# Optimization experiments

Measured on AMD Instinct MI355X. Metric: run time of the kernel, lower is better.

Reference implementation:

```python
import jax, jax.numpy as jnp
import numpy as np

N, D, P = 8192, 512, 3
TEMP, SIM_TH, DIS_TH, CLIP = 0.1, 0.15, 0.35, 30.0
NEG = -1e9  # finite stand-in for -inf mask (exp underflows to 0 identically)


def setup_inputs() -> dict:
    key = jax.random.key(0)
    k1, k2 = jax.random.split(key)
    embeddings = jax.random.normal(k1, (N, D), dtype=jnp.float32)
    thetas = jax.random.uniform(k2, (N, P), dtype=jnp.float32)
    return {"embeddings": embeddings, "thetas": thetas}


def reference(embeddings, thetas):
    n = embeddings.shape[0]
    # F.normalize(dim=-1)
    e = embeddings / jnp.maximum(
        jnp.linalg.norm(embeddings, axis=-1, keepdims=True), 1e-12)
    sim = jnp.clip(e @ e.T / TEMP, -CLIP, CLIP)  # [N, N]

    # cdist(thetas, thetas) normalized by its max; only feeds boolean masks
    t = jax.lax.stop_gradient(thetas)
    sq = jnp.sum(t * t, axis=1)
    d2 = jnp.maximum(sq[:, None] + sq[None, :] - 2.0 * (t @ t.T), 0.0)
    dist = jnp.sqrt(d2)
    dist = dist / (dist.max() + 1e-8)

    eye = jnp.eye(n, dtype=bool)
    pos = (dist < SIM_TH) & ~eye      # positives (self excluded: diag is -inf masked)
    neg = dist > DIS_TH               # negatives (diag never included: dist==0)
    sel = pos | neg

    # per-row cross_entropy over logits [pos_idx; neg_idx] with label 0 is:
    #   -sim[i, first_pos_index(i)] + logsumexp_{j in sel(i)} sim[i, j]
    masked = jnp.where(sel, sim, NEG)
    denom = jax.nn.logsumexp(masked, axis=1)            # [N]
    tgt = jnp.argmax(pos, axis=1)                       # first positive index
    tgt_logit = jnp.take_along_axis(sim, tgt[:, None], axis=1)[:, 0]
    valid = pos.any(axis=1) & neg.any(axis=1)
    per_row = jnp.where(valid, denom - tgt_logit, 0.0)
    cnt = valid.sum()
    return jnp.where(cnt > 0, per_row.sum() / jnp.maximum(cnt, 1), 0.0)
```

## Files before the change

kernel.cpp:

```cpp
#include <hip/hip_runtime.h>

#define N 8192
#define D 512

typedef __attribute__((ext_vector_type(4))) float f32x4;
typedef __attribute__((ext_vector_type(2))) long long2v;

typedef const __attribute__((address_space(1))) unsigned int* gas_t;
typedef __attribute__((address_space(3))) unsigned int* las_t;

static __device__ __forceinline__ void gl_lds16(const void* g, char* l) {
    __builtin_amdgcn_global_load_lds((gas_t)g, (las_t)l, 16, 0, 0);
}
static __device__ __forceinline__ int tri_cum(int r) { return r * (129 - r) / 2; }

static __device__ __forceinline__ unsigned f2fp8(float f) {
    unsigned u = __float_as_uint(f);
    unsigned sgn = (u >> 24) & 0x80u;
    unsigned a = u & 0x7FFFFFFFu;
    if (a >= 0x3C800000u) {
        unsigned t = a + 0x7FFFFu + ((a >> 20) & 1u);
        unsigned code = (((t >> 23) - 120u) << 3) | ((t >> 20) & 7u);
        if (code > 0x7Eu) code = 0x7Eu;
        return sgn | code;
    }
    float af = __uint_as_float(a);
    unsigned m = (unsigned)(af * 512.0f + 0.5f);
    return sgn | (m > 8u ? 8u : m);
}
static __device__ __forceinline__ float fp82f(unsigned c) {
    unsigned e = (c >> 3) & 15u, m = c & 7u;
    float v = (e == 0u) ? (float)m * 0.001953125f
                        : __uint_as_float(((e + 120u) << 23) | (m << 20));
    return (c & 0x80u) ? -v : v;
}

__global__ void knorm(const float* __restrict__ emb, unsigned char* __restrict__ e,
                      float* __restrict__ srow, unsigned* __restrict__ jminrow,
                      unsigned* __restrict__ negrow, unsigned* __restrict__ d2mb) {
    int w    = threadIdx.x >> 6;
    int row  = blockIdx.x * 4 + w;
    int lane = threadIdx.x & 63;
    const float4* src = (const float4*)(emb + (size_t)row * D);
    float4 v0 = src[lane * 2];
    float4 v1 = src[lane * 2 + 1];
    float ss = v0.x*v0.x + v0.y*v0.y + v0.z*v0.z + v0.w*v0.w
             + v1.x*v1.x + v1.y*v1.y + v1.z*v1.z + v1.w*v1.w;
#pragma unroll
    for (int off = 1; off < 64; off <<= 1) ss += __shfl_xor(ss, off, 64);
    float inv = 3.7982826f / fmaxf(sqrtf(ss), 1e-12f);
    unsigned c0 = f2fp8(v0.x * inv), c1 = f2fp8(v0.y * inv);
    unsigned c2 = f2fp8(v0.z * inv), c3 = f2fp8(v0.w * inv);
    unsigned c4 = f2fp8(v1.x * inv), c5 = f2fp8(v1.y * inv);
    unsigned c6 = f2fp8(v1.z * inv), c7 = f2fp8(v1.w * inv);
    uint2 pk;
    pk.x = c0 | (c1 << 8) | (c2 << 16) | (c3 << 24);
    pk.y = c4 | (c5 << 8) | (c6 << 16) | (c7 << 24);
    {
        int c = lane >> 3, u = lane & 7;
        int off8 = c * 64 + ((u < 4) ? u * 16 : (u - 4) * 16 + 8);
        *(uint2*)(e + (size_t)row * D + off8) = pk;
    }
    if (lane == 0) {
        srow[row] = 0.0f;
        jminrow[row] = 0xFFFFFFFFu;
        negrow[row] = 0u;
    }
    if (blockIdx.x == 0 && threadIdx.x == 0) *d2mb = 0u;
}

__global__ void kth(const float* __restrict__ th, float4* __restrict__ th4,
                    unsigned* __restrict__ d2mb) {
    int tid = threadIdx.x, bid = blockIdx.x;
    if (bid < 32) {
        int i = bid * 256 + tid;
        float x = th[3 * i], y = th[3 * i + 1], z = th[3 * i + 2];
        float4 v; v.x = x; v.y = y; v.z = z; v.w = x * x + y * y + z * z;
        th4[i] = v;
    }
    int w = tid >> 6, lane = tid & 63;
    int widx = bid * 4 + w;
    int q0 = widx * 4;
    int m0 = N - 4 - q0;
    float4 A[4], B[4];
#pragma unroll
    for (int k = 0; k < 4; k++) {
        float x = th[3 * (q0 + k)], y = th[3 * (q0 + k) + 1], z = th[3 * (q0 + k) + 2];
        A[k].x = x; A[k].y = y; A[k].z = z; A[k].w = x * x + y * y + z * z;
        x = th[3 * (m0 + k)]; y = th[3 * (m0 + k) + 1]; z = th[3 * (m0 + k) + 2];
        B[k].x = x; B[k].y = y; B[k].z = z; B[k].w = x * x + y * y + z * z;
    }
    float m = 0.0f;
    for (int j = q0 + 1 + lane; j < N; j += 64) {
        float x = th[3 * j], y = th[3 * j + 1], z = th[3 * j + 2];
        float tw = x * x + y * y + z * z;
        float d;
        d = A[0].w + tw - 2.0f * (A[0].x*x + A[0].y*y + A[0].z*z); m = fmaxf(m, d);
        d = A[1].w + tw - 2.0f * (A[1].x*x + A[1].y*y + A[1].z*z); m = fmaxf(m, d);
        d = A[2].w + tw - 2.0f * (A[2].x*x + A[2].y*y + A[2].z*z); m = fmaxf(m, d);
        d = A[3].w + tw - 2.0f * (A[3].x*x + A[3].y*y + A[3].z*z); m = fmaxf(m, d);
    }
    for (int j = m0 + 1 + lane; j < N; j += 64) {
        float x = th[3 * j], y = th[3 * j + 1], z = th[3 * j + 2];
        float tw = x * x + y * y + z * z;
        float d;
        d = B[0].w + tw - 2.0f * (B[0].x*x + B[0].y*y + B[0].z*z); m = fmaxf(m, d);
        d = B[1].w + tw - 2.0f * (B[1].x*x + B[1].y*y + B[1].z*z); m = fmaxf(m, d);
        d = B[2].w + tw - 2.0f * (B[2].x*x + B[2].y*y + B[2].z*z); m = fmaxf(m, d);
        d = B[3].w + tw - 2.0f * (B[3].x*x + B[3].y*y + B[3].z*z); m = fmaxf(m, d);
    }
#pragma unroll
    for (int off = 1; off < 64; off <<= 1) m = fmaxf(m, __shfl_xor(m, off, 64));
    __shared__ float red[4];
    if (lane == 0) red[w] = m;
    __syncthreads();
    if (tid == 0) {
        m = fmaxf(fmaxf(red[0], red[1]), fmaxf(red[2], red[3]));
        atomicMax(d2mb, __float_as_uint(m));
    }
}

__global__ __launch_bounds__(256) void kmain(
    const unsigned char* __restrict__ e, const float4* __restrict__ th4,
    const unsigned* __restrict__ d2mb, float* __restrict__ srow,
    unsigned* __restrict__ jminrow, unsigned* __restrict__ negrow) {
    __shared__ __align__(16) char smem[49152];

    const int tid  = threadIdx.x;
    const int lane = tid & 63;
    const int w    = tid >> 6;
    const int wr   = w >> 1;
    const int wc   = w & 1;

    const int bid = (int)blockIdx.x;
    const int swz = (bid & 7) * 260 + (bid >> 3);
    int rb = (int)((129.0f - sqrtf(16641.0f - 8.0f * (float)swz)) * 0.5f);
    rb = rb < 0 ? 0 : (rb > 63 ? 63 : rb);
    while (tri_cum(rb + 1) <= swz) rb++;
    while (tri_cum(rb) > swz) rb--;
    const int cb = rb + (swz - tri_cum(rb));
    const bool isdiag = (rb == cb);
    const int r0 = rb * 128, c0 = cb * 128;

    const int ssw = (((tid & 3) ^ ((tid >> 3) & 3)) << 4);
    const unsigned char* pA0 = e + (size_t)(r0 + (tid >> 2)) * D + ssw;
    const unsigned char* pA1 = pA0 + (size_t)64 * D;
    const unsigned char* pB0 = e + (size_t)(c0 + (tid >> 2)) * D + ssw;
    const unsigned char* pB1 = pB0 + (size_t)64 * D;

    const int fr = lane & 15;
    const int fq = lane >> 4;
    const int kslot = (fq ^ ((fr >> 1) & 3)) << 4;

    f32x4 acc[4][4];
#pragma unroll
    for (int mt = 0; mt < 4; mt++)
#pragma unroll
        for (int nt = 0; nt < 4; nt++) acc[mt][nt] = (f32x4){0.f, 0.f, 0.f, 0.f};

#define STAGE(T, BUF) { \
    const int k0_ = (T) * 64; char* d_ = smem + (BUF) * 16384;   \
    gl_lds16(pA0 + k0_, d_ + tid * 16);                          \
    gl_lds16(pA1 + k0_, d_ + 4096 + tid * 16);                   \
    gl_lds16(pB0 + k0_, d_ + 8192 + tid * 16);                   \
    gl_lds16(pB1 + k0_, d_ + 12288 + tid * 16); }

#define COMPUTE(BUF) { \
    const char* cA_ = smem + (BUF) * 16384;                      \
    const char* cB_ = cA_ + 8192;                                \
    long2v a_[4], b_[4];                                         \
    _Pragma("unroll")                                            \
    for (int mt = 0; mt < 4; mt++)                               \
        a_[mt] = *(const long2v*)(cA_ + (wr * 64 + mt * 16 + fr) * 64 + kslot); \
    _Pragma("unroll")                                            \
    for (int nt = 0; nt < 4; nt++)                               \
        b_[nt] = *(const long2v*)(cB_ + (wc * 64 + nt * 16 + fr) * 64 + kslot); \
    _Pragma("unroll")                                            \
    for (int mt = 0; mt < 4; mt++)                               \
    _Pragma("unroll")                                            \
    for (int nt = 0; nt < 4; nt++) {                             \
        acc[mt][nt] = __builtin_amdgcn_mfma_f32_16x16x32_fp8_fp8( \
            a_[mt][0], b_[nt][0], acc[mt][nt], 0, 0, 0);         \
        acc[mt][nt] = __builtin_amdgcn_mfma_f32_16x16x32_fp8_fp8( \
            a_[mt][1], b_[nt][1], acc[mt][nt], 0, 0, 0);         \
    } }

#define KST(WAITN, SBUF, DOSTAGE, ST, CBUF)                       \
    asm volatile("s_waitcnt vmcnt(" #WAITN ")" ::: "memory");     \
    __builtin_amdgcn_s_barrier();                                 \
    __builtin_amdgcn_sched_barrier(0);                            \
    if (DOSTAGE) STAGE(ST, SBUF)                                  \
    COMPUTE(CBUF)

    STAGE(0, 0)
    STAGE(1, 1)
    KST(4, 2, 1, 2, 0)
    KST(4, 0, 1, 3, 1)
    KST(4, 1, 1, 4, 2)
    KST(4, 2, 1, 5, 0)
    KST(4, 0, 1, 6, 1)
    KST(4, 1, 1, 7, 2)
    KST(4, 0, 0, 0, 0)
    KST(0, 0, 0, 0, 1)
#undef KST
#undef COMPUTE
#undef STAGE
    __syncthreads();

    const float dmax = sqrtf(__uint_as_float(*d2mb)) + 1e-8f;
    const float p2 = 0.0225f * dmax * dmax;
    const float n2 = 0.1225f * dmax * dmax;

    const int j0 = c0 + wc * 64 + fr;
    float4 thj[4];
#pragma unroll
    for (int nt = 0; nt < 4; nt++) thj[nt] = th4[j0 + nt * 16];

    float*    lds_rs = (float*)smem;
    unsigned* lds_rj = (unsigned*)(smem + 1024);
    unsigned* lds_rn = (unsigned*)(smem + 2048);
    float*    lds_cs = (float*)(smem + 3072);
    unsigned* lds_cj = (unsigned*)(smem + 4096);
    unsigned* lds_cn = (unsigned*)(smem + 5120);

    float    csum[4]; unsigned cjm[4], cng[4];
#pragma unroll
    for (int nt = 0; nt < 4; nt++) { csum[nt] = 0.0f; cjm[nt] = 0xFFFFFFFFu; cng[nt] = 0u; }

    const int i0 = r0 + wr * 64 + fq * 4;
#pragma unroll
    for (int mt = 0; mt < 4; mt++) {
#pragma unroll
        for (int rr = 0; rr < 4; rr++) {
            const int i = i0 + mt * 16 + rr;
            const float4 ti = th4[i];
            float sv = 0.0f; unsigned jv = 0xFFFFFFFFu, nv = 0u;
#pragma unroll
            for (int nt = 0; nt < 4; nt++) {
                const int j = j0 + nt * 16;
                const float4 tj = thj[nt];
                float dot = ti.x * tj.x + ti.y * tj.y + ti.z * tj.z;
                float d2 = fmaf(-2.0f, dot, ti.w + tj.w);
                bool pos = isdiag ? ((d2 < p2) && (j != i)) : (d2 < p2);
                bool neg = (d2 > n2);
                float c = (pos || neg) ? exp2f(acc[mt][nt][rr]) : 0.0f;
                sv += c;
                if (neg) nv = 1u;
                if (pos) jv = min(jv, (unsigned)j);
                if (!isdiag) {
                    csum[nt] += c;
                    if (neg) cng[nt] = 1u;
                    if (pos) cjm[nt] = min(cjm[nt], (unsigned)i);
                }
            }
#pragma unroll
            for (int off = 1; off < 16; off <<= 1) {
                sv += __shfl_xor(sv, off, 64);
                jv = min(jv, (unsigned)__shfl_xor((int)jv, off, 64));
                nv |= (unsigned)__shfl_xor((int)nv, off, 64);
            }
            if (fr == 0) {
                const int rl = wr * 64 + mt * 16 + fq * 4 + rr;
                lds_rs[wc * 128 + rl] = sv;
                lds_rj[wc * 128 + rl] = jv;
                lds_rn[wc * 128 + rl] = nv;
            }
        }
    }

    if (!isdiag) {
#pragma unroll
        for (int nt = 0; nt < 4; nt++) {
            float sv = csum[nt]; unsigned jv = cjm[nt], nv = cng[nt];
#pragma unroll
            for (int off = 16; off < 64; off <<= 1) {
                sv += __shfl_xor(sv, off, 64);
                jv = min(jv, (unsigned)__shfl_xor((int)jv, off, 64));
                nv |= (unsigned)__shfl_xor((int)nv, off, 64);
            }
            if (fq == 0) {
                const int cl = wc * 64 + nt * 16 + fr;
                lds_cs[wr * 128 + cl] = sv;
                lds_cj[wr * 128 + cl] = jv;
                lds_cn[wr * 128 + cl] = nv;
            }
        }
    }
    __syncthreads();
    if (tid < 128) {
        float    sv = lds_rs[tid] + lds_rs[128 + tid];
        unsigned jv = min(lds_rj[tid], lds_rj[128 + tid]);
        unsigned nv = lds_rn[tid] | lds_rn[128 + tid];
        atomicAdd(&srow[r0 + tid], sv);
        atomicMin(&jminrow[r0 + tid], jv);
        atomicOr(&negrow[r0 + tid], nv);
        if (!isdiag) {
            float    cv = lds_cs[tid] + lds_cs[128 + tid];
            unsigned cj = min(lds_cj[tid], lds_cj[128 + tid]);
            unsigned cn = lds_cn[tid] | lds_cn[128 + tid];
            atomicAdd(&srow[c0 + tid], cv);
            atomicMin(&jminrow[c0 + tid], cj);
            atomicOr(&negrow[c0 + tid], cn);
        }
    }
}

__global__ void krow(const unsigned char* __restrict__ e, const float* __restrict__ srow,
                     const unsigned* __restrict__ jminrow, const unsigned* __restrict__ negrow,
                     float* __restrict__ pr, float* __restrict__ vf) {
    int row  = blockIdx.x * 4 + (threadIdx.x >> 6);
    int lane = threadIdx.x & 63;
    unsigned jmv = jminrow[row];
    bool valid = (jmv != 0xFFFFFFFFu) && (negrow[row] != 0u);
    float p = 0.0f;
    if (valid) {
        const uint2* a = (const uint2*)(e + (size_t)row * D);
        const uint2* b = (const uint2*)(e + (size_t)jmv * D);
        uint2 va = a[lane], vb = b[lane];
        float dot = 0.0f;
#pragma unroll
        for (int k = 0; k < 4; k++)
            dot += fp82f((va.x >> (8 * k)) & 0xFFu) * fp82f((vb.x >> (8 * k)) & 0xFFu);
#pragma unroll
        for (int k = 0; k < 4; k++)
            dot += fp82f((va.y >> (8 * k)) & 0xFFu) * fp82f((vb.y >> (8 * k)) & 0xFFu);
#pragma unroll
        for (int off = 1; off < 64; off <<= 1) dot += __shfl_xor(dot, off, 64);
        p = logf(srow[row]) - dot * 0.69314718f;
    }
    if (lane == 0) { pr[row] = p; vf[row] = valid ? 1.0f : 0.0f; }
}

__global__ void kfinal(const float* __restrict__ pr, const float* __restrict__ vf,
                       float* __restrict__ out) {
    __shared__ float ls[1024];
    __shared__ float lc[1024];
    int t = threadIdx.x;
    float sv = 0.0f, cv = 0.0f;
#pragma unroll
    for (int k = 0; k < 8; k++) { sv += pr[t * 8 + k]; cv += vf[t * 8 + k]; }
    ls[t] = sv; lc[t] = cv;
    __syncthreads();
    for (int off = 512; off > 0; off >>= 1) {
        if (t < off) { ls[t] += ls[t + off]; lc[t] += lc[t + off]; }
        __syncthreads();
    }
    if (t == 0) out[0] = (lc[0] > 0.0f) ? (ls[0] / lc[0]) : 0.0f;
}

extern "C" void kernel_launch(void* const* d_in, const int* in_sizes, int n_in,
                              void* d_out, int out_size, void* d_ws, size_t ws_size,
                              hipStream_t stream) {
    const float* emb = (const float*)d_in[0];
    const float* th  = (const float*)d_in[1];
    float* out = (float*)d_out;
    char* ws = (char*)d_ws;

    unsigned char* e     = (unsigned char*)(ws);
    float4*   th4        = (float4*)(ws + 8388608);
    float*    srow       = (float*)(ws + 8519680);
    unsigned* jminr      = (unsigned*)(ws + 8552448);
    unsigned* negr       = (unsigned*)(ws + 8585216);
    float*    pr         = (float*)(ws + 8617984);
    float*    vf         = (float*)(ws + 8650752);
    unsigned* d2mb       = (unsigned*)(ws + 8683520);

    knorm<<<N / 4, 256, 0, stream>>>(emb, e, srow, jminr, negr, d2mb);
    kth<<<256, 256, 0, stream>>>(th, th4, d2mb);
    kmain<<<2080, 256, 0, stream>>>(e, th4, d2mb, srow, jminr, negr);
    krow<<<N / 4, 256, 0, stream>>>(e, srow, jminr, negr, pr, vf);
    kfinal<<<1, 1024, 0, stream>>>(pr, vf, out);
}
```

Before: 110.9 us.

## Use 512-thread blocks with 2x4 wave grid in main similarity kernel

The main fused GEMM/mask kernel moves from 4 to 8 waves per 128x128 tile. Each wave now computes a 64x32 sub-tile instead of 64x64, so there are half as many accumulators per wave. Each thread issues two global-to-LDS loads per stage instead of four. The reduction layout and the atomic flush are reworked for the 2x4 wave grid, with row and column flushes split across different thread groups. The goal is more latency hiding and parallel epilogue work, at the cost of more LDS reads of the A fragments per MFMA and larger blocks.

```diff
diff --git a/kernel.cpp b/kernel.cpp
--- a/kernel.cpp
+++ b/kernel.cpp
@@ -120,7 +120,7 @@
     }
 }
 
-__global__ __launch_bounds__(256) void kmain(
+__global__ __launch_bounds__(512) void kmain(
     const unsigned char* __restrict__ e, const float4* __restrict__ th4,
     const unsigned* __restrict__ d2mb, float* __restrict__ srow,
     unsigned* __restrict__ jminrow, unsigned* __restrict__ negrow) {
@@ -129,8 +129,8 @@
     const int tid  = threadIdx.x;
     const int lane = tid & 63;
     const int w    = tid >> 6;
-    const int wr   = w >> 1;
-    const int wc   = w & 1;
+    const int wr   = w >> 2;
+    const int wc   = w & 3;
 
     const int bid = (int)blockIdx.x;
     const int swz = (bid & 7) * 260 + (bid >> 3);
@@ -143,42 +143,38 @@
     const int r0 = rb * 128, c0 = cb * 128;
 
     const int ssw = (((tid & 3) ^ ((tid >> 3) & 3)) << 4);
-    const unsigned char* pA0 = e + (size_t)(r0 + (tid >> 2)) * D + ssw;
-    const unsigned char* pA1 = pA0 + (size_t)64 * D;
-    const unsigned char* pB0 = e + (size_t)(c0 + (tid >> 2)) * D + ssw;
-    const unsigned char* pB1 = pB0 + (size_t)64 * D;
+    const unsigned char* pA = e + (size_t)(r0 + (tid >> 2)) * D + ssw;
+    const unsigned char* pB = e + (size_t)(c0 + (tid >> 2)) * D + ssw;
 
     const int fr = lane & 15;
     const int fq = lane >> 4;
     const int kslot = (fq ^ ((fr >> 1) & 3)) << 4;
 
-    f32x4 acc[4][4];
+    f32x4 acc[4][2];
 #pragma unroll
     for (int mt = 0; mt < 4; mt++)
 #pragma unroll
-        for (int nt = 0; nt < 4; nt++) acc[mt][nt] = (f32x4){0.f, 0.f, 0.f, 0.f};
+        for (int nt = 0; nt < 2; nt++) acc[mt][nt] = (f32x4){0.f, 0.f, 0.f, 0.f};
 
 #define STAGE(T, BUF) { \
     const int k0_ = (T) * 64; char* d_ = smem + (BUF) * 16384;   \
-    gl_lds16(pA0 + k0_, d_ + tid * 16);                          \
-    gl_lds16(pA1 + k0_, d_ + 4096 + tid * 16);                   \
-    gl_lds16(pB0 + k0_, d_ + 8192 + tid * 16);                   \
-    gl_lds16(pB1 + k0_, d_ + 12288 + tid * 16); }
+    gl_lds16(pA + k0_, d_ + tid * 16);                           \
+    gl_lds16(pB + k0_, d_ + 8192 + tid * 16); }
 
 #define COMPUTE(BUF) { \
     const char* cA_ = smem + (BUF) * 16384;                      \
     const char* cB_ = cA_ + 8192;                                \
-    long2v a_[4], b_[4];                                         \
+    long2v a_[4], b_[2];                                         \
     _Pragma("unroll")                                            \
     for (int mt = 0; mt < 4; mt++)                               \
         a_[mt] = *(const long2v*)(cA_ + (wr * 64 + mt * 16 + fr) * 64 + kslot); \
     _Pragma("unroll")                                            \
-    for (int nt = 0; nt < 4; nt++)                               \
-        b_[nt] = *(const long2v*)(cB_ + (wc * 64 + nt * 16 + fr) * 64 + kslot); \
+    for (int nt = 0; nt < 2; nt++)                               \
+        b_[nt] = *(const long2v*)(cB_ + (wc * 32 + nt * 16 + fr) * 64 + kslot); \
     _Pragma("unroll")                                            \
     for (int mt = 0; mt < 4; mt++)                               \
     _Pragma("unroll")                                            \
-    for (int nt = 0; nt < 4; nt++) {                             \
+    for (int nt = 0; nt < 2; nt++) {                             \
         acc[mt][nt] = __builtin_amdgcn_mfma_f32_16x16x32_fp8_fp8( \
             a_[mt][0], b_[nt][0], acc[mt][nt], 0, 0, 0);         \
         acc[mt][nt] = __builtin_amdgcn_mfma_f32_16x16x32_fp8_fp8( \
@@ -194,13 +190,13 @@
 
     STAGE(0, 0)
     STAGE(1, 1)
-    KST(4, 2, 1, 2, 0)
-    KST(4, 0, 1, 3, 1)
-    KST(4, 1, 1, 4, 2)
-    KST(4, 2, 1, 5, 0)
-    KST(4, 0, 1, 6, 1)
-    KST(4, 1, 1, 7, 2)
-    KST(4, 0, 0, 0, 0)
+    KST(2, 2, 1, 2, 0)
+    KST(2, 0, 1, 3, 1)
+    KST(2, 1, 1, 4, 2)
+    KST(2, 2, 1, 5, 0)
+    KST(2, 0, 1, 6, 1)
+    KST(2, 1, 1, 7, 2)
+    KST(2, 0, 0, 0, 0)
     KST(0, 0, 0, 0, 1)
 #undef KST
 #undef COMPUTE
@@ -211,21 +207,21 @@
     const float p2 = 0.0225f * dmax * dmax;
     const float n2 = 0.1225f * dmax * dmax;
 
-    const int j0 = c0 + wc * 64 + fr;
-    float4 thj[4];
-#pragma unroll
-    for (int nt = 0; nt < 4; nt++) thj[nt] = th4[j0 + nt * 16];
+    const int j0 = c0 + wc * 32 + fr;
+    float4 thj[2];
+#pragma unroll
+    for (int nt = 0; nt < 2; nt++) thj[nt] = th4[j0 + nt * 16];
 
     float*    lds_rs = (float*)smem;
-    unsigned* lds_rj = (unsigned*)(smem + 1024);
-    unsigned* lds_rn = (unsigned*)(smem + 2048);
-    float*    lds_cs = (float*)(smem + 3072);
-    unsigned* lds_cj = (unsigned*)(smem + 4096);
-    unsigned* lds_cn = (unsigned*)(smem + 5120);
-
-    float    csum[4]; unsigned cjm[4], cng[4];
-#pragma unroll
-    for (int nt = 0; nt < 4; nt++) { csum[nt] = 0.0f; cjm[nt] = 0xFFFFFFFFu; cng[nt] = 0u; }
+    unsigned* lds_rj = (unsigned*)(smem + 2048);
+    unsigned* lds_rn = (unsigned*)(smem + 4096);
+    float*    lds_cs = (float*)(smem + 6144);
+    unsigned* lds_cj = (unsigned*)(smem + 7168);
+    unsigned* lds_cn = (unsigned*)(smem + 8192);
+
+    float    csum[2]; unsigned cjm[2], cng[2];
+#pragma unroll
+    for (int nt = 0; nt < 2; nt++) { csum[nt] = 0.0f; cjm[nt] = 0xFFFFFFFFu; cng[nt] = 0u; }
 
     const int i0 = r0 + wr * 64 + fq * 4;
 #pragma unroll
@@ -236,7 +232,7 @@
             const float4 ti = th4[i];
             float sv = 0.0f; unsigned jv = 0xFFFFFFFFu, nv = 0u;
 #pragma unroll
-            for (int nt = 0; nt < 4; nt++) {
+            for (int nt = 0; nt < 2; nt++) {
                 const int j = j0 + nt * 16;
                 const float4 tj = thj[nt];
                 float dot = ti.x * tj.x + ti.y * tj.y + ti.z * tj.z;
@@ -270,7 +266,7 @@
 
     if (!isdiag) {
 #pragma unroll
-        for (int nt = 0; nt < 4; nt++) {
+        for (int nt = 0; nt < 2; nt++) {
             float sv = csum[nt]; unsigned jv = cjm[nt], nv = cng[nt];
 #pragma unroll
             for (int off = 16; off < 64; off <<= 1) {
@@ -279,7 +275,7 @@
                 nv |= (unsigned)__shfl_xor((int)nv, off, 64);
             }
             if (fq == 0) {
-                const int cl = wc * 64 + nt * 16 + fr;
+                const int cl = wc * 32 + nt * 16 + fr;
                 lds_cs[wr * 128 + cl] = sv;
                 lds_cj[wr * 128 + cl] = jv;
                 lds_cn[wr * 128 + cl] = nv;
@@ -288,20 +284,21 @@
     }
     __syncthreads();
     if (tid < 128) {
-        float    sv = lds_rs[tid] + lds_rs[128 + tid];
-        unsigned jv = min(lds_rj[tid], lds_rj[128 + tid]);
-        unsigned nv = lds_rn[tid] | lds_rn[128 + tid];
+        float    sv = lds_rs[tid] + lds_rs[128 + tid] + lds_rs[256 + tid] + lds_rs[384 + tid];
+        unsigned jv = min(min(lds_rj[tid], lds_rj[128 + tid]),
+                          min(lds_rj[256 + tid], lds_rj[384 + tid]));
+        unsigned nv = lds_rn[tid] | lds_rn[128 + tid] | lds_rn[256 + tid] | lds_rn[384 + tid];
         atomicAdd(&srow[r0 + tid], sv);
         atomicMin(&jminrow[r0 + tid], jv);
         atomicOr(&negrow[r0 + tid], nv);
-        if (!isdiag) {
-            float    cv = lds_cs[tid] + lds_cs[128 + tid];
-            unsigned cj = min(lds_cj[tid], lds_cj[128 + tid]);
-            unsigned cn = lds_cn[tid] | lds_cn[128 + tid];
-            atomicAdd(&srow[c0 + tid], cv);
-            atomicMin(&jminrow[c0 + tid], cj);
-            atomicOr(&negrow[c0 + tid], cn);
-        }
+    } else if (tid < 256 && !isdiag) {
+        const int t2 = tid - 128;
+        float    cv = lds_cs[t2] + lds_cs[128 + t2];
+        unsigned cj = min(lds_cj[t2], lds_cj[128 + t2]);
+        unsigned cn = lds_cn[t2] | lds_cn[128 + t2];
+        atomicAdd(&srow[c0 + t2], cv);
+        atomicMin(&jminrow[c0 + t2], cj);
+        atomicOr(&negrow[c0 + t2], cn);
     }
 }
 
@@ -367,7 +364,7 @@
 
     knorm<<<N / 4, 256, 0, stream>>>(emb, e, srow, jminr, negr, d2mb);
     kth<<<256, 256, 0, stream>>>(th, th4, d2mb);
-    kmain<<<2080, 256, 0, stream>>>(e, th4, d2mb, srow, jminr, negr);
+    kmain<<<2080, 512, 0, stream>>>(e, th4, d2mb, srow, jminr, negr);
     krow<<<N / 4, 256, 0, stream>>>(e, srow, jminr, negr, pr, vf);
     kfinal<<<1, 1024, 0, stream>>>(pr, vf, out);
 }
```

Result: slower. 130.6 us (+17.8%).
